# Performance work log

Hardware: AMD Instinct MI355X
Metric: run time of the kernel (lower is better)

The kernel has to match this reference:

```python
import jax, jax.numpy as jnp
import numpy as np

N_FEATURES = 4096
IN_DIM = 4096
BATCH = 4096
NNZ = int(0.01 * N_FEATURES * IN_DIM)  # 167772, matches sparse_coo_init


def setup_inputs() -> dict:
    key = jax.random.key(0)
    k_in, k_vals, k_rows, k_cols, k_bias = jax.random.split(key, 5)
    inputs = jax.random.normal(k_in, (BATCH, IN_DIM), dtype=jnp.float32)
    kernel_vals = jax.random.normal(k_vals, (NNZ,), dtype=jnp.float32)
    kernel_rows = jax.random.randint(k_rows, (NNZ,), 0, N_FEATURES, dtype=jnp.int32)
    kernel_cols = jax.random.randint(k_cols, (NNZ,), 0, IN_DIM, dtype=jnp.int32)
    bias = jax.random.normal(k_bias, (N_FEATURES,), dtype=jnp.float32)
    return {
        "inputs": inputs,
        "kernel_vals": kernel_vals,
        "kernel_rows": kernel_rows,
        "kernel_cols": kernel_cols,
        "bias": bias,
    }


def reference(inputs, kernel_vals, kernel_rows, kernel_cols, bias):
    # COO sparse-dense matmul: A (n_features x in_dim, COO with duplicate-
    # index summation) @ inputs.T, then transpose and add bias:
    #   z = (A @ inputs.T).T + bias  ==  inputs @ A.T + bias
    # Densifying the small (4096x4096 = 64MB) kernel via scatter-add is the
    # memory-cheapest faithful form (avoids an nnz x batch intermediate) and
    # exactly reproduces COO semantics (duplicates sum).
    dense_kernel = jnp.zeros((N_FEATURES, IN_DIM), dtype=kernel_vals.dtype)
    dense_kernel = dense_kernel.at[kernel_rows, kernel_cols].add(kernel_vals)
    # [batch, in_dim] @ [in_dim, n_features] -> [batch, n_features]
    z = jnp.einsum('bd,fd->bf', inputs, dense_kernel) + bias
    return z
```

## Files before the change

kernel.cpp:

```cpp
#include <hip/hip_runtime.h>
#include <hip/hip_fp16.h>


#define NF 4096
#define IND 4096
#define BATCH_TOTAL 4096
#define FT 16
#define BT 512
#define NT_MAIN 512
#define NPHASE 4
#define NKEYS (NPHASE * NF)
#define NTILES ((IND / 64) * (BATCH_TOTAL / 64))

typedef float f32x4 __attribute__((ext_vector_type(4)));

__device__ __forceinline__ float bf2f(unsigned short u) {
    return __uint_as_float(((unsigned int)u) << 16);
}
__device__ __forceinline__ unsigned short f2bf(float x) {
    unsigned int h = __float_as_uint(x);
    h += 0x7fff + ((h >> 16) & 1);
    return (unsigned short)(h >> 16);
}

__global__ __launch_bounds__(256)
void fused_transpose_hist(const float* __restrict__ in,
                          __half* __restrict__ outT,
                          const int* __restrict__ rows,
                          const int* __restrict__ cols,
                          int* __restrict__ cntq, int nnz) {
    if (blockIdx.x < NTILES) {
        __shared__ float t[64][65];
        const int tb = blockIdx.x;
        const int d0 = (tb & 63) * 64;
        const int b0 = (tb >> 6) * 64;
        const int tx4 = threadIdx.x & 15;
        const int ty  = threadIdx.x >> 4;
#pragma unroll
        for (int p = 0; p < 4; ++p) {
            int brow = ty + p * 16;
            float4 v = *(const float4*)(in + (long)(b0 + brow) * IND + d0 + tx4 * 4);
            t[brow][tx4 * 4 + 0] = v.x;
            t[brow][tx4 * 4 + 1] = v.y;
            t[brow][tx4 * 4 + 2] = v.z;
            t[brow][tx4 * 4 + 3] = v.w;
        }
        __syncthreads();
        const int bx4 = threadIdx.x & 15;
        const int dy  = threadIdx.x >> 4;
#pragma unroll
        for (int p = 0; p < 4; ++p) {
            int drow = dy + p * 16;
            __half h4[4];
            h4[0] = __float2half(t[bx4 * 4 + 0][drow]);
            h4[1] = __float2half(t[bx4 * 4 + 1][drow]);
            h4[2] = __float2half(t[bx4 * 4 + 2][drow]);
            h4[3] = __float2half(t[bx4 * 4 + 3][drow]);
            *(ushort4*)(outT + (long)(d0 + drow) * BATCH_TOTAL + b0 + bx4 * 4) =
                *(const ushort4*)h4;
        }
    } else {
        int k = (blockIdx.x - NTILES) * 256 + threadIdx.x;
        if (k < nnz) {
            int key = ((cols[k] >> 10) << 12) | rows[k];
            atomicAdd(&cntq[key], 1);
        }
    }
}

__global__ __launch_bounds__(512)
void scan16k_kernel(const int* __restrict__ cntq, int2* __restrict__ seg,
                    int* __restrict__ cursorq) {
    __shared__ int ts[512];
    const int t = threadIdx.x;
    const int base = t * 32;
    int e[32];
    int tot = 0;
#pragma unroll
    for (int i = 0; i < 32; ++i) { e[i] = cntq[base + i]; tot += e[i]; }
    ts[t] = tot;
    __syncthreads();
    for (int off = 1; off < 512; off <<= 1) {
        int v = (t >= off) ? ts[t - off] : 0;
        __syncthreads();
        ts[t] += v;
        __syncthreads();
    }
    int run = (t == 0) ? 0 : ts[t - 1];
#pragma unroll
    for (int i = 0; i < 32; ++i) {
        seg[base + i] = make_int2(run, e[i]);
        cursorq[base + i] = run;
        run += e[i];
    }
}

__global__ void scatter_pairsq_kernel(const float* __restrict__ vals,
                                      const int* __restrict__ rows,
                                      const int* __restrict__ cols,
                                      int* __restrict__ cursorq,
                                      int2* __restrict__ pairs, int nnz) {
    int k = blockIdx.x * blockDim.x + threadIdx.x;
    if (k < nnz) {
        int c = cols[k];
        int key = ((c >> 10) << 12) | rows[k];
        int p = atomicAdd(&cursorq[key], 1);
        pairs[p] = make_int2(c, __float_as_int(vals[k]));
    }
}

__device__ __forceinline__ void upd(const int2 e,
                                    const __half* __restrict__ gbase,
                                    float* __restrict__ a) {
    float v = __int_as_float(e.y);
    union { uint4 u; __half h[8]; } U;
    U.u = *(const uint4*)(gbase + (long)e.x * BATCH_TOTAL);
#pragma unroll
    for (int j = 0; j < 8; ++j)
        a[j] += v * __half2float(U.h[j]);
}

__global__ __launch_bounds__(NT_MAIN, 8)
void spmm_axpy_kernel(const __half* __restrict__ inT,
                      const int2* __restrict__ pairs,
                      const int2* __restrict__ seg,
                      const float* __restrict__ bias,
                      float* __restrict__ out) {
#pragma clang fp contract(fast)
    __shared__ unsigned short tile[FT][BT + 8];

    const int bid = blockIdx.x;
    const int per = gridDim.x >> 3;
    const int wg = (bid & 7) * per + (bid >> 3);
    const int fblk = wg & (NF / FT - 1);
    const int bt   = wg >> 8;
    const int b0 = bt * BT;
    const int fbase = fblk * FT;

    const int tid = threadIdx.x;
    const int wid = tid >> 6;
    const int lane = tid & 63;

    const int fA = fbase + wid;
    const int fB = fbase + 8 + wid;

    int sA[NPHASE], nA[NPHASE], sB[NPHASE], nB[NPHASE];
#pragma unroll
    for (int h = 0; h < NPHASE; ++h) {
        int2 dA = seg[h * NF + fA];
        int2 dB = seg[h * NF + fB];
        sA[h] = __builtin_amdgcn_readfirstlane(dA.x);
        nA[h] = __builtin_amdgcn_readfirstlane(dA.y);
        sB[h] = __builtin_amdgcn_readfirstlane(dB.x);
        nB[h] = __builtin_amdgcn_readfirstlane(dB.y);
    }

    float aA[8] = {0.f, 0.f, 0.f, 0.f, 0.f, 0.f, 0.f, 0.f};
    float aB[8] = {0.f, 0.f, 0.f, 0.f, 0.f, 0.f, 0.f, 0.f};
    const __half* gbase = inT + b0 + lane * 8;

#pragma unroll
    for (int h = 0; h < NPHASE; ++h) {
        const int m = min(nA[h], nB[h]);
#pragma unroll 2
        for (int k = 0; k < m; ++k) {
            int2 eA = pairs[sA[h] + k];
            int2 eB = pairs[sB[h] + k];
            upd(eA, gbase, aA);
            upd(eB, gbase, aB);
        }
        for (int k = m; k < nA[h]; ++k) upd(pairs[sA[h] + k], gbase, aA);
        for (int k = m; k < nB[h]; ++k) upd(pairs[sB[h] + k], gbase, aB);
    }

    ushort4 p0, p1;
    p0.x = f2bf(aA[0]); p0.y = f2bf(aA[1]); p0.z = f2bf(aA[2]); p0.w = f2bf(aA[3]);
    p1.x = f2bf(aA[4]); p1.y = f2bf(aA[5]); p1.z = f2bf(aA[6]); p1.w = f2bf(aA[7]);
    *(ushort4*)(&tile[wid][lane * 8])     = p0;
    *(ushort4*)(&tile[wid][lane * 8 + 4]) = p1;
    p0.x = f2bf(aB[0]); p0.y = f2bf(aB[1]); p0.z = f2bf(aB[2]); p0.w = f2bf(aB[3]);
    p1.x = f2bf(aB[4]); p1.y = f2bf(aB[5]); p1.z = f2bf(aB[6]); p1.w = f2bf(aB[7]);
    *(ushort4*)(&tile[wid + 8][lane * 8])     = p0;
    *(ushort4*)(&tile[wid + 8][lane * 8 + 4]) = p1;
    __syncthreads();

    const int chunk = tid & 3;
    const int rbase = tid >> 2;
    float4 bv = ((const float4*)bias)[(fbase >> 2) + chunk];
#pragma unroll
    for (int p = 0; p < 4; ++p) {
        int r = rbase + p * 128;
        f32x4 o;
        o.x = bf2f(tile[chunk * 4 + 0][r]) + bv.x;
        o.y = bf2f(tile[chunk * 4 + 1][r]) + bv.y;
        o.z = bf2f(tile[chunk * 4 + 2][r]) + bv.z;
        o.w = bf2f(tile[chunk * 4 + 3][r]) + bv.w;
        __builtin_nontemporal_store(
            o, (f32x4*)(out + (long)(b0 + r) * NF + fbase + chunk * 4));
    }
}

__global__ void init_out_kernel(float* __restrict__ out,
                                const float* __restrict__ bias) {
    const int nf4 = NF / 4;
    const long total = (long)BATCH_TOTAL * nf4;
    const float4* b4 = (const float4*)bias;
    float4* o4 = (float4*)out;
    for (long i = (long)blockIdx.x * blockDim.x + threadIdx.x; i < total;
         i += (long)gridDim.x * blockDim.x)
        o4[i] = b4[i & (nf4 - 1)];
}

__global__ void hist_kernel(const int* __restrict__ rows,
                            int* __restrict__ cnt, int nnz) {
    int k = blockIdx.x * blockDim.x + threadIdx.x;
    if (k < nnz) atomicAdd(&cnt[rows[k]], 1);
}

__global__ __launch_bounds__(1024)
void scan_kernel(const int* __restrict__ cnt, int* __restrict__ rptr,
                 int* __restrict__ cursor) {
    __shared__ int ts[1024];
    const int t = threadIdx.x;
    const int base = t * 4;
    int e0 = cnt[base], e1 = cnt[base + 1], e2 = cnt[base + 2], e3 = cnt[base + 3];
    ts[t] = e0 + e1 + e2 + e3;
    __syncthreads();
    for (int off = 1; off < 1024; off <<= 1) {
        int v = (t >= off) ? ts[t - off] : 0;
        __syncthreads();
        ts[t] += v;
        __syncthreads();
    }
    int excl = (t == 0) ? 0 : ts[t - 1];
    int p0 = excl, p1 = excl + e0, p2 = p1 + e1, p3 = p2 + e2;
    rptr[base + 0] = p0;   cursor[base + 0] = p0;
    rptr[base + 1] = p1;   cursor[base + 1] = p1;
    rptr[base + 2] = p2;   cursor[base + 2] = p2;
    rptr[base + 3] = p3;   cursor[base + 3] = p3;
}

__global__ void scatter3_kernel(const float* __restrict__ vals,
                                const int* __restrict__ rows,
                                const int* __restrict__ cols,
                                int* __restrict__ cursor,
                                float* __restrict__ sval,
                                int* __restrict__ scol,
                                int* __restrict__ srow, int nnz) {
    int k = blockIdx.x * blockDim.x + threadIdx.x;
    if (k < nnz) {
        int r = rows[k];
        int p = atomicAdd(&cursor[r], 1);
        sval[p] = vals[k];
        scol[p] = cols[k];
        srow[p] = r;
    }
}

#define TILE_B_FB 4
__global__ __launch_bounds__(512, 4)
void spmm_csr_fb_kernel(const float* __restrict__ inputs,
                        const float* __restrict__ sval,
                        const int* __restrict__ scol,
                        const int* __restrict__ srow,
                        float* __restrict__ out, int nnz) {
    __shared__ float in_lds[TILE_B_FB][IND];
    const int tid = threadIdx.x;
    const long b0 = (long)blockIdx.x * TILE_B_FB;
    for (int i = tid; i < IND / 4; i += 512) {
#pragma unroll
        for (int j = 0; j < TILE_B_FB; ++j)
            ((float4*)in_lds[j])[i] = ((const float4*)(inputs + (b0 + j) * IND))[i];
    }
    __syncthreads();
    const int C = (nnz + 511) / 512;
    int k0 = tid * C, k1 = min(k0 + C, nnz);
    if (k0 < k1) {
        int cur = srow[k0];
        float a0 = 0.f, a1 = 0.f, a2 = 0.f, a3 = 0.f;
        for (int k = k0; k < k1; ++k) {
            int r = srow[k];
            float v = sval[k];
            int c = scol[k];
            if (r != cur) {
                atomicAdd(&out[(b0 + 0) * NF + cur], a0);
                atomicAdd(&out[(b0 + 1) * NF + cur], a1);
                atomicAdd(&out[(b0 + 2) * NF + cur], a2);
                atomicAdd(&out[(b0 + 3) * NF + cur], a3);
                a0 = a1 = a2 = a3 = 0.f;
                cur = r;
            }
            a0 += v * in_lds[0][c];
            a1 += v * in_lds[1][c];
            a2 += v * in_lds[2][c];
            a3 += v * in_lds[3][c];
        }
        atomicAdd(&out[(b0 + 0) * NF + cur], a0);
        atomicAdd(&out[(b0 + 1) * NF + cur], a1);
        atomicAdd(&out[(b0 + 2) * NF + cur], a2);
        atomicAdd(&out[(b0 + 3) * NF + cur], a3);
    }
}

extern "C" void kernel_launch(void* const* d_in, const int* in_sizes, int n_in,
                              void* d_out, int out_size, void* d_ws, size_t ws_size,
                              hipStream_t stream) {
    const float* inputs = (const float*)d_in[0];
    const float* vals   = (const float*)d_in[1];
    const int*   rows   = (const int*)d_in[2];
    const int*   cols   = (const int*)d_in[3];
    const float* bias   = (const float*)d_in[4];
    float* out = (float*)d_out;
    const int nnz = in_sizes[1];

    char* ws = (char*)d_ws;
    size_t off = 0;
    int*  cntq    = (int*)(ws + off);  off += (size_t)NKEYS * 4;
    int*  cursorq = (int*)(ws + off);  off += (size_t)NKEYS * 4;
    int2* seg     = (int2*)(ws + off); off += (size_t)NKEYS * 8;
    size_t pairs_off = (off + 15) & ~(size_t)15;
    int2* pairs = (int2*)(ws + pairs_off);
    size_t after_pairs = (pairs_off + (size_t)nnz * 8 + 15) & ~(size_t)15;
    __half* inT = (__half*)(ws + after_pairs);
    size_t need_main = after_pairs + (size_t)IND * BATCH_TOTAL * 2;

    const int eb = (nnz + 255) / 256;

    if (need_main <= ws_size) {
        (void)hipMemsetAsync(cntq, 0, (size_t)NKEYS * 4, stream);
        fused_transpose_hist<<<NTILES + eb, 256, 0, stream>>>(
            inputs, inT, rows, cols, cntq, nnz);
        scan16k_kernel<<<1, 512, 0, stream>>>(cntq, seg, cursorq);
        scatter_pairsq_kernel<<<eb, 256, 0, stream>>>(vals, rows, cols, cursorq,
                                                      pairs, nnz);
        spmm_axpy_kernel<<<(NF / FT) * (BATCH_TOTAL / BT), NT_MAIN, 0, stream>>>(
            inT, pairs, seg, bias, out);
    } else {
        int* cnt    = cntq;
        int* cursor = cursorq;
        int* rptr   = (int*)seg;
        int*   srow = (int*)(ws + pairs_off);
        int*   scol = srow + nnz;
        float* sval = (float*)(scol + nnz);
        (void)hipMemsetAsync(cnt, 0, (size_t)NF * 4, stream);
        init_out_kernel<<<2048, 256, 0, stream>>>(out, bias);
        hist_kernel<<<eb, 256, 0, stream>>>(rows, cnt, nnz);
        scan_kernel<<<1, 1024, 0, stream>>>(cnt, rptr, cursor);
        scatter3_kernel<<<eb, 256, 0, stream>>>(vals, rows, cols, cursor,
                                                sval, scol, srow, nnz);
        spmm_csr_fb_kernel<<<BATCH_TOTAL / TILE_B_FB, 512, 0, stream>>>(
            inputs, sval, scol, srow, out, nnz);
    }
}
```

Before: 120.9 us.

## Double the SpMM batch tile so each lane accumulates sixteen outputs

Batch tile width grows from 512 to 1024 columns, so each lane now holds 16 accumulators per feature and loads two 16-byte fp16 vectors per nonzero. Each (value, column) pair is fetched half as often and per-block segment setup is amortised over more work, at the cost of half as many blocks and more registers per thread. The interleaved A/B pair loop is replaced by separate sequential segment walks, which removes the tail loops but may give up some memory-level parallelism. The 16K-entry scan kernel also switches its count loads to int4 vector loads.

```diff
diff --git a/kernel.cpp b/kernel.cpp
--- a/kernel.cpp
+++ b/kernel.cpp
@@ -6,7 +6,7 @@
 #define IND 4096
 #define BATCH_TOTAL 4096
 #define FT 16
-#define BT 512
+#define BT 1024
 #define NT_MAIN 512
 #define NPHASE 4
 #define NKEYS (NPHASE * NF)
@@ -75,9 +75,12 @@
     const int t = threadIdx.x;
     const int base = t * 32;
     int e[32];
+#pragma unroll
+    for (int i = 0; i < 8; ++i)
+        *(int4*)&e[i * 4] = *(const int4*)&cntq[base + i * 4];
     int tot = 0;
 #pragma unroll
-    for (int i = 0; i < 32; ++i) { e[i] = cntq[base + i]; tot += e[i]; }
+    for (int i = 0; i < 32; ++i) tot += e[i];
     ts[t] = tot;
     __syncthreads();
     for (int off = 1; off < 512; off <<= 1) {
@@ -109,15 +112,24 @@
     }
 }
 
-__device__ __forceinline__ void upd(const int2 e,
-                                    const __half* __restrict__ gbase,
-                                    float* __restrict__ a) {
-    float v = __int_as_float(e.y);
-    union { uint4 u; __half h[8]; } U;
-    U.u = *(const uint4*)(gbase + (long)e.x * BATCH_TOTAL);
-#pragma unroll
-    for (int j = 0; j < 8; ++j)
-        a[j] += v * __half2float(U.h[j]);
+__device__ __forceinline__ void walk_seg(const int2* __restrict__ pairs,
+                                         int start, int n,
+                                         const __half* __restrict__ gbase,
+                                         float* __restrict__ a) {
+    for (int k = 0; k < n; ++k) {
+        int2 e = pairs[start + k];
+        float v = __int_as_float(e.y);
+        const __half* g = gbase + (long)e.x * BATCH_TOTAL;
+        union { uint4 u; __half h[8]; } U0, U1;
+        U0.u = *(const uint4*)(g);
+        U1.u = *(const uint4*)(g + 8);
+#pragma unroll
+        for (int j = 0; j < 8; ++j)
+            a[j] += v * __half2float(U0.h[j]);
+#pragma unroll
+        for (int j = 0; j < 8; ++j)
+            a[8 + j] += v * __half2float(U1.h[j]);
+    }
 }
 
 __global__ __launch_bounds__(NT_MAIN, 8)
@@ -155,40 +167,45 @@
         nB[h] = __builtin_amdgcn_readfirstlane(dB.y);
     }
 
-    float aA[8] = {0.f, 0.f, 0.f, 0.f, 0.f, 0.f, 0.f, 0.f};
-    float aB[8] = {0.f, 0.f, 0.f, 0.f, 0.f, 0.f, 0.f, 0.f};
-    const __half* gbase = inT + b0 + lane * 8;
+    float aA[16], aB[16];
+#pragma unroll
+    for (int j = 0; j < 16; ++j) { aA[j] = 0.f; aB[j] = 0.f; }
+    const __half* gbase = inT + b0 + lane * 16;
 
 #pragma unroll
     for (int h = 0; h < NPHASE; ++h) {
-        const int m = min(nA[h], nB[h]);
-#pragma unroll 2
-        for (int k = 0; k < m; ++k) {
-            int2 eA = pairs[sA[h] + k];
-            int2 eB = pairs[sB[h] + k];
-            upd(eA, gbase, aA);
-            upd(eB, gbase, aB);
-        }
-        for (int k = m; k < nA[h]; ++k) upd(pairs[sA[h] + k], gbase, aA);
-        for (int k = m; k < nB[h]; ++k) upd(pairs[sB[h] + k], gbase, aB);
-    }
-
-    ushort4 p0, p1;
-    p0.x = f2bf(aA[0]); p0.y = f2bf(aA[1]); p0.z = f2bf(aA[2]); p0.w = f2bf(aA[3]);
-    p1.x = f2bf(aA[4]); p1.y = f2bf(aA[5]); p1.z = f2bf(aA[6]); p1.w = f2bf(aA[7]);
-    *(ushort4*)(&tile[wid][lane * 8])     = p0;
-    *(ushort4*)(&tile[wid][lane * 8 + 4]) = p1;
-    p0.x = f2bf(aB[0]); p0.y = f2bf(aB[1]); p0.z = f2bf(aB[2]); p0.w = f2bf(aB[3]);
-    p1.x = f2bf(aB[4]); p1.y = f2bf(aB[5]); p1.z = f2bf(aB[6]); p1.w = f2bf(aB[7]);
-    *(ushort4*)(&tile[wid + 8][lane * 8])     = p0;
-    *(ushort4*)(&tile[wid + 8][lane * 8 + 4]) = p1;
+        walk_seg(pairs, sA[h], nA[h], gbase, aA);
+        walk_seg(pairs, sB[h], nB[h], gbase, aB);
+    }
+
+    ushort4 q[4];
+#pragma unroll
+    for (int j = 0; j < 4; ++j) {
+        q[j].x = f2bf(aA[j * 4 + 0]);
+        q[j].y = f2bf(aA[j * 4 + 1]);
+        q[j].z = f2bf(aA[j * 4 + 2]);
+        q[j].w = f2bf(aA[j * 4 + 3]);
+    }
+#pragma unroll
+    for (int j = 0; j < 4; ++j)
+        *(ushort4*)(&tile[wid][lane * 16 + j * 4]) = q[j];
+#pragma unroll
+    for (int j = 0; j < 4; ++j) {
+        q[j].x = f2bf(aB[j * 4 + 0]);
+        q[j].y = f2bf(aB[j * 4 + 1]);
+        q[j].z = f2bf(aB[j * 4 + 2]);
+        q[j].w = f2bf(aB[j * 4 + 3]);
+    }
+#pragma unroll
+    for (int j = 0; j < 4; ++j)
+        *(ushort4*)(&tile[wid + 8][lane * 16 + j * 4]) = q[j];
     __syncthreads();
 
     const int chunk = tid & 3;
     const int rbase = tid >> 2;
     float4 bv = ((const float4*)bias)[(fbase >> 2) + chunk];
 #pragma unroll
-    for (int p = 0; p < 4; ++p) {
+    for (int p = 0; p < 8; ++p) {
         int r = rbase + p * 128;
         f32x4 o;
         o.x = bf2f(tile[chunk * 4 + 0][r]) + bv.x;
```

After: 133.2 us. +10.2%, slower.
